# Optimization experiments

Measured on AMD Instinct MI355X. Metric: run time of the kernel, lower is better.

Reference implementation:

```python
import jax, jax.numpy as jnp
from jax import lax
import numpy as np

L, D, HEADS, DH, FF = 12, 768, 12, 64, 3072
PATCH, IMG, B, S, OUT = 16, 224, 32, 197, 512


def setup_inputs() -> dict:
    key = jax.random.key(0)
    ks = jax.random.split(key, 10)
    nrm = lambda k, shp, s=0.02: jax.random.normal(k, shp, jnp.float32) * s
    return {
        "x_inp": jax.random.normal(ks[0], (B, 3, IMG, IMG), jnp.float32),
        "conv_w": nrm(ks[1], (D, 3, PATCH, PATCH)),
        "cls_emb": nrm(ks[2], (D,)),
        "pos_emb": nrm(ks[3], (S, D)),
        "ln_pre_w": jnp.ones((D,), jnp.float32),
        "ln_pre_b": jnp.zeros((D,), jnp.float32),
        "ln1_w": jnp.ones((L, D), jnp.float32),
        "ln1_b": jnp.zeros((L, D), jnp.float32),
        "qkv_w": nrm(ks[4], (L, 3 * D, D)),
        "qkv_b": jnp.zeros((L, 3 * D), jnp.float32),
        "out_w": nrm(ks[5], (L, D, D)),
        "out_b": jnp.zeros((L, D), jnp.float32),
        "ln2_w": jnp.ones((L, D), jnp.float32),
        "ln2_b": jnp.zeros((L, D), jnp.float32),
        "fc1_w": nrm(ks[6], (L, FF, D)),
        "fc1_b": jnp.zeros((L, FF), jnp.float32),
        "fc2_w": nrm(ks[7], (L, D, FF)),
        "fc2_b": jnp.zeros((L, D), jnp.float32),
        "ln_post_w": jnp.ones((D,), jnp.float32),
        "ln_post_b": jnp.zeros((D,), jnp.float32),
        "proj": nrm(ks[8], (D, OUT)),
    }


def _ln(x, w, b, eps=1e-5):
    mu = jnp.mean(x, axis=-1, keepdims=True)
    var = jnp.mean(jnp.square(x - mu), axis=-1, keepdims=True)
    return (x - mu) * lax.rsqrt(var + eps) * w + b


def _visual_forward(x_inp, conv_w, cls_emb, pos_emb, ln_pre_w, ln_pre_b,
                    ln1_w, ln1_b, qkv_w, qkv_b, out_w, out_b,
                    ln2_w, ln2_b, fc1_w, fc1_b, fc2_w, fc2_b,
                    ln_post_w, ln_post_b, proj):
    # patch embedding: conv stride=patch, no bias  -> [B, D, 14, 14]
    x = lax.conv_general_dilated(x_inp, conv_w, (PATCH, PATCH), 'VALID',
                                 dimension_numbers=('NCHW', 'OIHW', 'NCHW'))
    b = x.shape[0]
    x = x.reshape(b, D, -1).transpose(0, 2, 1)              # [B, 196, D]
    cls = jnp.broadcast_to(cls_emb, (b, 1, D))
    x = jnp.concatenate([cls, x], axis=1)                   # [B, 197, D]
    x = x + pos_emb[None]                                   # standard 197-token branch
    x = _ln(x, ln_pre_w, ln_pre_b)

    scale = float(DH) ** -0.5

    def block(h, p):
        l1w, l1b, qw, qb, ow, ob, l2w, l2b, f1w, f1b, f2w, f2b = p
        y = _ln(h, l1w, l1b)
        qkv = y @ qw.T + qb                                  # [B, S, 3D]
        q, k, v = jnp.split(qkv, 3, axis=-1)
        q = q.reshape(b, S, HEADS, DH) * scale
        k = k.reshape(b, S, HEADS, DH)
        v = v.reshape(b, S, HEADS, DH)
        attn = jnp.einsum('bqhd,bkhd->bhqk', q, k)
        attn = jax.nn.softmax(attn, axis=-1)
        o = jnp.einsum('bhqk,bkhd->bqhd', attn, v).reshape(b, S, D)
        h = h + o @ ow.T + ob
        y = _ln(h, l2w, l2b)
        y = y @ f1w.T + f1b
        y = y * jax.nn.sigmoid(1.702 * y)                    # QuickGELU
        h = h + y @ f2w.T + f2b
        return h, None

    params = (ln1_w, ln1_b, qkv_w, qkv_b, out_w, out_b,
              ln2_w, ln2_b, fc1_w, fc1_b, fc2_w, fc2_b)
    x, _ = lax.scan(block, x, params)

    cls_out = _ln(x[:, 0, :], ln_post_w, ln_post_b)
    return cls_out @ proj                                    # [B, 512]


def reference(x_inp, conv_w, cls_emb, pos_emb, ln_pre_w, ln_pre_b,
              ln1_w, ln1_b, qkv_w, qkv_b, out_w, out_b,
              ln2_w, ln2_b, fc1_w, fc1_b, fc2_w, fc2_b,
              ln_post_w, ln_post_b, proj):
    return _visual_forward(x_inp, conv_w, cls_emb, pos_emb, ln_pre_w, ln_pre_b,
                           ln1_w, ln1_b, qkv_w, qkv_b, out_w, out_b,
                           ln2_w, ln2_b, fc1_w, fc1_b, fc2_w, fc2_b,
                           ln_post_w, ln_post_b, proj)
```

## Files before the change

kernel.cpp:

```cpp
#include <hip/hip_runtime.h>
#include <hip/hip_bf16.h>


#define LAYERS 12
#define DMODEL 768
#define NHEADS 12
#define DHEAD  64
#define FFDIM  3072
#define BATCH  32
#define SEQ    197
#define NPATCH 196
#define OUTD   512
#define MROWS  (BATCH * SEQ)
#define MPAD   6400
#define SPAD   208
#define VSTR   208

typedef __attribute__((ext_vector_type(4))) float f32x4;
typedef __attribute__((ext_vector_type(8))) short bf16x8;

enum { M_F32 = 0, M_ACC = 1, M_GELU = 2, M_PATCH = 3, M_QKVB = 4 };

__device__ __forceinline__ float b2f(short s) {
    unsigned u = ((unsigned)(unsigned short)s) << 16;
    return __builtin_bit_cast(float, u);
}
__device__ __forceinline__ short f2b(float f) {
    __hip_bfloat16 h = __float2bfloat16(f);
    return __builtin_bit_cast(short, h);
}
__device__ __forceinline__ unsigned short f2bu(float f) {
    __hip_bfloat16 h = __float2bfloat16(f);
    return __builtin_bit_cast(unsigned short, h);
}

__device__ __forceinline__ void gl2lds16(const void* g, void* l) {
    __builtin_amdgcn_global_load_lds(
        (const __attribute__((address_space(1))) void*)g,
        (__attribute__((address_space(3))) void*)l, 16, 0, 0);
}

__global__ __launch_bounds__(256) void cvt_bf16_kernel(
    const float* __restrict__ src, __hip_bfloat16* __restrict__ dst, long n)
{
    long i0 = ((long)blockIdx.x * 256 + threadIdx.x) * 4;
    long stride = (long)gridDim.x * 1024;
    for (long i = i0; i < n; i += stride) {
        float4 v = *reinterpret_cast<const float4*>(&src[i]);
        dst[i + 0] = __float2bfloat16(v.x);
        dst[i + 1] = __float2bfloat16(v.y);
        dst[i + 2] = __float2bfloat16(v.z);
        dst[i + 3] = __float2bfloat16(v.w);
    }
}

__global__ __launch_bounds__(256) void im2col_kernel(
    const float* __restrict__ x_inp, __hip_bfloat16* __restrict__ patches)
{
    int bp = blockIdx.x;
    int b = bp / NPATCH, p = bp % NPATCH;
    int py = p / 14, px = p % 14;
    const float* xb = x_inp + (long)b * 3 * 224 * 224;
    for (int e = threadIdx.x; e < 768; e += 256) {
        int c = e >> 8, i = (e >> 4) & 15, j = e & 15;
        patches[(long)bp * 768 + e] =
            __float2bfloat16(xb[((long)c * 224 + py * 16 + i) * 224 + px * 16 + j]);
    }
}

__global__ __launch_bounds__(256) void cls_token_kernel(
    const float* __restrict__ cls_emb, const float* __restrict__ pos_emb,
    float* __restrict__ x)
{
    int b = blockIdx.x;
    for (int d = threadIdx.x; d < DMODEL; d += 256)
        x[(long)b * SEQ * DMODEL + d] = cls_emb[d] + pos_emb[d];
}

template<int OB>
__global__ __launch_bounds__(256) void ln_kernel(
    const float* __restrict__ in, void* __restrict__ out,
    const float* __restrict__ w, const float* __restrict__ bb,
    long in_stride, long out_stride, int nrows)
{
    int row = blockIdx.x * 4 + (threadIdx.x >> 6);
    if (row >= nrows) return;
    int lane = threadIdx.x & 63;
    const float* xr = in + (long)row * in_stride;

    float4 v[3];
    float s = 0.f;
    #pragma unroll
    for (int i = 0; i < 3; ++i) {
        v[i] = *reinterpret_cast<const float4*>(&xr[i * 256 + lane * 4]);
        s += v[i].x + v[i].y + v[i].z + v[i].w;
    }
    #pragma unroll
    for (int off = 32; off; off >>= 1) s += __shfl_xor(s, off);
    float mean = s * (1.0f / DMODEL);
    float sq = 0.f;
    #pragma unroll
    for (int i = 0; i < 3; ++i) {
        float a = v[i].x - mean, b2 = v[i].y - mean,
              c = v[i].z - mean, d = v[i].w - mean;
        sq += a * a + b2 * b2 + c * c + d * d;
    }
    #pragma unroll
    for (int off = 32; off; off >>= 1) sq += __shfl_xor(sq, off);
    float rstd = rsqrtf(sq * (1.0f / DMODEL) + 1e-5f);

    #pragma unroll
    for (int i = 0; i < 3; ++i) {
        int d0 = i * 256 + lane * 4;
        float4 wv = *reinterpret_cast<const float4*>(&w[d0]);
        float4 bv = *reinterpret_cast<const float4*>(&bb[d0]);
        float o0 = (v[i].x - mean) * rstd * wv.x + bv.x;
        float o1 = (v[i].y - mean) * rstd * wv.y + bv.y;
        float o2 = (v[i].z - mean) * rstd * wv.z + bv.z;
        float o3 = (v[i].w - mean) * rstd * wv.w + bv.w;
        if (OB) {
            ushort4 u;
            u.x = f2bu(o0); u.y = f2bu(o1); u.z = f2bu(o2); u.w = f2bu(o3);
            *reinterpret_cast<ushort4*>(
                &((__hip_bfloat16*)out)[(long)row * out_stride + d0]) = u;
        } else {
            float4 o = make_float4(o0, o1, o2, o3);
            *reinterpret_cast<float4*>(&((float*)out)[(long)row * out_stride + d0]) = o;
        }
    }
}

template<int MODE>
__global__ __launch_bounds__(256) void gemm_bf16(
    const __hip_bfloat16* __restrict__ A, const __hip_bfloat16* __restrict__ W,
    const float* __restrict__ bias, float* __restrict__ Cf,
    __hip_bfloat16* __restrict__ Cb, int M, int N, int K, int NB,
    const float* __restrict__ pos)
{
    __shared__ short As[2][64 * 64];
    __shared__ short Bs[2][128 * 64];
    int tid = threadIdx.x, lane = tid & 63, wv = tid >> 6;

    int nwg = gridDim.x, bid = blockIdx.x;
    int qq = nwg >> 3, rr = nwg & 7;
    int xcd = bid & 7, idx = bid >> 3;
    int newid = (xcd < rr ? xcd * (qq + 1) : rr * (qq + 1) + (xcd - rr) * qq) + idx;

    int bm = (newid / NB) * 64, bn = (newid % NB) * 128;
    int wn = wv * 32;
    f32x4 acc[4][2] = {};

    int sr = tid >> 3, sc = tid & 7;
    int c_log = sc ^ (sr & 7);
    const short* Ag = (const short*)A + (long)(bm + sr) * K + (c_log << 3);
    const short* Bg = (const short*)W + (long)(bn + sr) * K + (c_log << 3);
    const long K32 = (long)32 * K;

    int lg = lane >> 4, lr16 = lane & 15;
    int aoff[2][4], boff[2][2];
    #pragma unroll
    for (int s = 0; s < 2; ++s) {
        #pragma unroll
        for (int i = 0; i < 4; ++i) {
            int ra = i * 16 + lr16;
            aoff[s][i] = (ra << 6) + ((((s << 2) | lg) ^ (ra & 7)) << 3);
        }
        #pragma unroll
        for (int j = 0; j < 2; ++j) {
            int rb = wn + j * 16 + lr16;
            boff[s][j] = (rb << 6) + ((((s << 2) | lg) ^ (rb & 7)) << 3);
        }
    }

    const int KT = K >> 6;
    {
        char* Ad = (char*)&As[0][0]; char* Bd = (char*)&Bs[0][0];
        gl2lds16(Ag,           Ad + tid * 16);
        gl2lds16(Ag + K32,     Ad + 4096 + tid * 16);
        gl2lds16(Bg,           Bd + tid * 16);
        gl2lds16(Bg + K32,     Bd + 4096 + tid * 16);
        gl2lds16(Bg + 2 * K32, Bd + 8192 + tid * 16);
        gl2lds16(Bg + 3 * K32, Bd + 12288 + tid * 16);
    }
    __syncthreads();

    for (int t = 0; t < KT; ++t) {
        if (t + 1 < KT) {
            int ktn = (t + 1) << 6;
            char* Ad = (char*)&As[(t & 1) ^ 1][0];
            char* Bd = (char*)&Bs[(t & 1) ^ 1][0];
            gl2lds16(Ag + ktn,           Ad + tid * 16);
            gl2lds16(Ag + K32 + ktn,     Ad + 4096 + tid * 16);
            gl2lds16(Bg + ktn,           Bd + tid * 16);
            gl2lds16(Bg + K32 + ktn,     Bd + 4096 + tid * 16);
            gl2lds16(Bg + 2 * K32 + ktn, Bd + 8192 + tid * 16);
            gl2lds16(Bg + 3 * K32 + ktn, Bd + 12288 + tid * 16);
        }
        const short* Ab = &As[t & 1][0];
        const short* Bb = &Bs[t & 1][0];
        #pragma unroll
        for (int s = 0; s < 2; ++s) {
            bf16x8 af[4], bfr[2];
            #pragma unroll
            for (int i = 0; i < 4; ++i)
                af[i] = *reinterpret_cast<const bf16x8*>(&Ab[aoff[s][i]]);
            #pragma unroll
            for (int j = 0; j < 2; ++j)
                bfr[j] = *reinterpret_cast<const bf16x8*>(&Bb[boff[s][j]]);
            #pragma unroll
            for (int mi = 0; mi < 4; ++mi)
                #pragma unroll
                for (int ni = 0; ni < 2; ++ni)
                    acc[mi][ni] = __builtin_amdgcn_mfma_f32_16x16x32_bf16(
                        af[mi], bfr[ni], acc[mi][ni], 0, 0, 0);
        }
        __syncthreads();
    }

    #pragma unroll
    for (int mi = 0; mi < 4; ++mi) {
        int row0 = bm + mi * 16 + (lane >> 4) * 4;
        #pragma unroll
        for (int ni = 0; ni < 2; ++ni) {
            int col = bn + wn + ni * 16 + lr16;
            #pragma unroll
            for (int r = 0; r < 4; ++r) {
                int row = row0 + r;
                if (row >= M) continue;
                float v = acc[mi][ni][r];
                if (MODE == M_PATCH) {
                    int pb = row / 196, pp = row - pb * 196;
                    Cf[((long)(pb * SEQ + 1 + pp)) * DMODEL + col] =
                        v + pos[(long)(1 + pp) * DMODEL + col];
                } else {
                    v += bias[col];
                    long idx2 = (long)row * N + col;
                    if (MODE == M_F32)      Cf[idx2] = v;
                    else if (MODE == M_ACC) Cf[idx2] += v;
                    else if (MODE == M_QKVB) Cb[idx2] = __float2bfloat16(v);
                    else if (MODE == M_GELU)
                        Cb[idx2] = __float2bfloat16(v / (1.f + __expf(-1.702f * v)));
                }
            }
        }
    }
}

__global__ __launch_bounds__(256) void attn_kernel(
    const __hip_bfloat16* __restrict__ qkv, __hip_bfloat16* __restrict__ o)
{
    int bh = blockIdx.x;
    int b = bh / NHEADS, h = bh % NHEADS;
    int tid = threadIdx.x, lane = tid & 63, wv = tid >> 6;
    __shared__ short Ks[SPAD * 64];
    __shared__ short Vt[64 * VSTR];
    __shared__ short Ps[4][16 * VSTR];
    const short* base = (const short*)qkv + (long)b * SEQ * 2304;

    for (int idx = tid; idx < SPAD * 8; idx += 256) {
        int r = idx >> 3, c = idx & 7;
        int4 val = make_int4(0, 0, 0, 0);
        if (r < SEQ)
            val = *reinterpret_cast<const int4*>(base + (long)r * 2304 + 768 + h * 64 + c * 8);
        *reinterpret_cast<int4*>(&Ks[r * 64 + ((c ^ (r & 7)) << 3)]) = val;
    }
    for (int idx = tid; idx < SPAD * 64; idx += 256) {
        int k = idx >> 6, d = idx & 63;
        short v = (k < SEQ) ? base[(long)k * 2304 + 1536 + h * 64 + d] : (short)0;
        Vt[d * VSTR + k] = v;
    }
    __syncthreads();

    int lg = lane >> 4, lr = lane & 15;
    short* Pw = Ps[wv];

    for (int ch = wv; ch < 13; ch += 4) {
        int q0 = ch * 16;
        const short* qp = (const short*)qkv +
            ((long)(b * SEQ) + q0 + lr) * 2304 + h * 64 + (lg << 3);
        bf16x8 qa = *reinterpret_cast<const bf16x8*>(qp);
        bf16x8 qb = *reinterpret_cast<const bf16x8*>(qp + 32);

        f32x4 sc[13];
        #pragma unroll
        for (int f = 0; f < 13; ++f) sc[f] = (f32x4){0.f, 0.f, 0.f, 0.f};
        #pragma unroll
        for (int f = 0; f < 13; ++f) {
            int row = f * 16 + lr;
            int sw = row & 7;
            const short* kr = &Ks[row * 64];
            bf16x8 k0 = *reinterpret_cast<const bf16x8*>(&kr[((lg + 0) ^ sw) << 3]);
            bf16x8 k1 = *reinterpret_cast<const bf16x8*>(&kr[((lg + 4) ^ sw) << 3]);
            sc[f] = __builtin_amdgcn_mfma_f32_16x16x32_bf16(qa, k0, sc[f], 0, 0, 0);
            sc[f] = __builtin_amdgcn_mfma_f32_16x16x32_bf16(qb, k1, sc[f], 0, 0, 0);
        }

        float mrow[4] = {-1e30f, -1e30f, -1e30f, -1e30f};
        #pragma unroll
        for (int f = 0; f < 13; ++f) {
            bool ok = f * 16 + lr < SEQ;
            #pragma unroll
            for (int r = 0; r < 4; ++r)
                if (ok) mrow[r] = fmaxf(mrow[r], sc[f][r] * 0.125f);
        }
        #pragma unroll
        for (int r = 0; r < 4; ++r)
            #pragma unroll
            for (int off = 8; off; off >>= 1)
                mrow[r] = fmaxf(mrow[r], __shfl_xor(mrow[r], off));
        float esum[4] = {0.f, 0.f, 0.f, 0.f};
        #pragma unroll
        for (int f = 0; f < 13; ++f) {
            bool ok = f * 16 + lr < SEQ;
            #pragma unroll
            for (int r = 0; r < 4; ++r) {
                float e = ok ? __expf(sc[f][r] * 0.125f - mrow[r]) : 0.f;
                sc[f][r] = e;
                esum[r] += e;
            }
        }
        #pragma unroll
        for (int r = 0; r < 4; ++r)
            #pragma unroll
            for (int off = 8; off; off >>= 1)
                esum[r] += __shfl_xor(esum[r], off);
        float inv[4];
        #pragma unroll
        for (int r = 0; r < 4; ++r) inv[r] = 1.0f / esum[r];

        #pragma unroll
        for (int f = 0; f < 13; ++f)
            #pragma unroll
            for (int r = 0; r < 4; ++r)
                Pw[(lg * 4 + r) * VSTR + f * 16 + lr] = f2b(sc[f][r] * inv[r]);

        f32x4 oa[4] = {};
        #pragma unroll
        for (int ks = 0; ks < 7; ++ks) {
            int kb = ks * 32 + (lg << 3);
            bf16x8 pa = {};
            if (kb < SPAD) pa = *reinterpret_cast<const bf16x8*>(&Pw[lr * VSTR + kb]);
            #pragma unroll
            for (int d = 0; d < 4; ++d) {
                bf16x8 vb = {};
                if (kb < SPAD)
                    vb = *reinterpret_cast<const bf16x8*>(&Vt[(d * 16 + lr) * VSTR + kb]);
                oa[d] = __builtin_amdgcn_mfma_f32_16x16x32_bf16(pa, vb, oa[d], 0, 0, 0);
            }
        }

        #pragma unroll
        for (int d = 0; d < 4; ++d)
            #pragma unroll
            for (int r = 0; r < 4; ++r) {
                int q = q0 + lg * 4 + r;
                if (q < SEQ)
                    o[((long)(b * SEQ + q)) * DMODEL + h * 64 + d * 16 + lr] =
                        __float2bfloat16(oa[d][r]);
            }
    }
}

__global__ __launch_bounds__(256) void proj_kernel(
    const float* __restrict__ cls_ln, const float* __restrict__ proj,
    float* __restrict__ out)
{
    int idx = blockIdx.x * 256 + threadIdx.x;
    int m = idx >> 9, n = idx & 511;
    float s = 0.f;
    #pragma unroll 8
    for (int k = 0; k < 768; ++k)
        s += cls_ln[m * 768 + k] * proj[k * 512 + n];
    out[idx] = s;
}

extern "C" void kernel_launch(void* const* d_in, const int* in_sizes, int n_in,
                              void* d_out, int out_size, void* d_ws, size_t ws_size,
                              hipStream_t stream) {
    const float* x_inp    = (const float*)d_in[0];
    const float* conv_w   = (const float*)d_in[1];
    const float* cls_emb  = (const float*)d_in[2];
    const float* pos_emb  = (const float*)d_in[3];
    const float* ln_pre_w = (const float*)d_in[4];
    const float* ln_pre_b = (const float*)d_in[5];
    const float* ln1_w    = (const float*)d_in[6];
    const float* ln1_b    = (const float*)d_in[7];
    const float* qkv_w    = (const float*)d_in[8];
    const float* qkv_b    = (const float*)d_in[9];
    const float* out_w    = (const float*)d_in[10];
    const float* out_b    = (const float*)d_in[11];
    const float* ln2_w    = (const float*)d_in[12];
    const float* ln2_b    = (const float*)d_in[13];
    const float* fc1_w    = (const float*)d_in[14];
    const float* fc1_b    = (const float*)d_in[15];
    const float* fc2_w    = (const float*)d_in[16];
    const float* fc2_b    = (const float*)d_in[17];
    const float* ln_post_w= (const float*)d_in[18];
    const float* ln_post_b= (const float*)d_in[19];
    const float* proj     = (const float*)d_in[20];

    char* w = (char*)d_ws;
    __hip_bfloat16* wqkv = (__hip_bfloat16*)w; w += (size_t)LAYERS * 2304 * DMODEL * 2;
    __hip_bfloat16* wout = (__hip_bfloat16*)w; w += (size_t)LAYERS * DMODEL * DMODEL * 2;
    __hip_bfloat16* wfc1 = (__hip_bfloat16*)w; w += (size_t)LAYERS * FFDIM * DMODEL * 2;
    __hip_bfloat16* wfc2 = (__hip_bfloat16*)w; w += (size_t)LAYERS * DMODEL * FFDIM * 2;
    __hip_bfloat16* wconv= (__hip_bfloat16*)w; w += (size_t)DMODEL * DMODEL * 2;
    float* x             = (float*)w;          w += (size_t)MROWS * DMODEL * 4;
    __hip_bfloat16* y    = (__hip_bfloat16*)w; w += (size_t)MPAD * DMODEL * 2;
    __hip_bfloat16* qkvb = (__hip_bfloat16*)w; w += (size_t)MPAD * 2304 * 2;
    __hip_bfloat16* attno= (__hip_bfloat16*)w; w += (size_t)MPAD * DMODEL * 2;
    __hip_bfloat16* h1   = (__hip_bfloat16*)w; w += (size_t)MPAD * FFDIM * 2;
    __hip_bfloat16* patches = (__hip_bfloat16*)w; w += (size_t)NPATCH * BATCH * DMODEL * 2;
    float* clsb          = (float*)w;          w += (size_t)BATCH * DMODEL * 4;

    cvt_bf16_kernel<<<2048, 256, 0, stream>>>(qkv_w, wqkv, (long)LAYERS * 2304 * DMODEL);
    cvt_bf16_kernel<<<2048, 256, 0, stream>>>(out_w, wout, (long)LAYERS * DMODEL * DMODEL);
    cvt_bf16_kernel<<<2048, 256, 0, stream>>>(fc1_w, wfc1, (long)LAYERS * FFDIM * DMODEL);
    cvt_bf16_kernel<<<2048, 256, 0, stream>>>(fc2_w, wfc2, (long)LAYERS * DMODEL * FFDIM);
    cvt_bf16_kernel<<<512, 256, 0, stream>>>(conv_w, wconv, (long)DMODEL * DMODEL);

    im2col_kernel<<<NPATCH * BATCH, 256, 0, stream>>>(x_inp, patches);
    gemm_bf16<M_PATCH><<<98 * 6, 256, 0, stream>>>(
        patches, wconv, nullptr, x, nullptr, NPATCH * BATCH, DMODEL, DMODEL, 6, pos_emb);
    cls_token_kernel<<<BATCH, 256, 0, stream>>>(cls_emb, pos_emb, x);
    ln_kernel<0><<<MROWS / 4, 256, 0, stream>>>(x, x, ln_pre_w, ln_pre_b,
                                                DMODEL, DMODEL, MROWS);

    for (int l = 0; l < LAYERS; ++l) {
        ln_kernel<1><<<MROWS / 4, 256, 0, stream>>>(x, y, ln1_w + l * DMODEL,
                                                    ln1_b + l * DMODEL, DMODEL, DMODEL, MROWS);
        gemm_bf16<M_QKVB><<<99 * 18, 256, 0, stream>>>(
            y, wqkv + (long)l * 2304 * DMODEL, qkv_b + (long)l * 2304, nullptr, qkvb,
            MROWS, 2304, DMODEL, 18, nullptr);
        attn_kernel<<<BATCH * NHEADS, 256, 0, stream>>>(qkvb, attno);
        gemm_bf16<M_ACC><<<99 * 6, 256, 0, stream>>>(
            attno, wout + (long)l * DMODEL * DMODEL, out_b + (long)l * DMODEL, x, nullptr,
            MROWS, DMODEL, DMODEL, 6, nullptr);
        ln_kernel<1><<<MROWS / 4, 256, 0, stream>>>(x, y, ln2_w + l * DMODEL,
                                                    ln2_b + l * DMODEL, DMODEL, DMODEL, MROWS);
        gemm_bf16<M_GELU><<<99 * 24, 256, 0, stream>>>(
            y, wfc1 + (long)l * FFDIM * DMODEL, fc1_b + (long)l * FFDIM, nullptr, h1,
            MROWS, FFDIM, DMODEL, 24, nullptr);
        gemm_bf16<M_ACC><<<99 * 6, 256, 0, stream>>>(
            h1, wfc2 + (long)l * DMODEL * FFDIM, fc2_b + (long)l * DMODEL, x, nullptr,
            MROWS, DMODEL, FFDIM, 6, nullptr);
    }

    ln_kernel<0><<<8, 256, 0, stream>>>(x, clsb, ln_post_w, ln_post_b,
                                        (long)SEQ * DMODEL, DMODEL, BATCH);
    proj_kernel<<<(BATCH * OUTD) / 256, 256, 0, stream>>>(clsb, proj, (float*)d_out);
}
```

Baseline: 3.404 ms.

## Add 128x128-tile GEMM with XCD-aware block remap for QKV and FC1

Adds a gemm128 kernel that uses 128x128 output tiles with a 64-wide K step, XOR-swizzled LDS and direct global-to-LDS loads. It also remaps block IDs so consecutive tiles land on the same XCD. The QKV and FC1 projections now use it in place of the previous 64-row-tile GEMM. The goal is more data reuse per loaded tile and better L2 locality on the large-N GEMMs. The trade-off is fewer workgroups, padding waste at M=6304 against 6400 rows, and higher register pressure from a 4x4 accumulator per wave.

```diff
diff --git a/kernel.cpp b/kernel.cpp
--- a/kernel.cpp
+++ b/kernel.cpp
@@ -241,6 +241,93 @@
                     else if (MODE == M_GELU)
                         Cb[idx2] = __float2bfloat16(v / (1.f + __expf(-1.702f * v)));
                 }
+            }
+        }
+    }
+}
+
+template<int MODE>
+__global__ __launch_bounds__(256) void gemm128(
+    const __hip_bfloat16* __restrict__ A, const __hip_bfloat16* __restrict__ W,
+    const float* __restrict__ bias, __hip_bfloat16* __restrict__ Cb,
+    int M, int N, int K, int NB)
+{
+    __shared__ short As[128 * 64];
+    __shared__ short Bs[128 * 64];
+    int tid = threadIdx.x, lane = tid & 63, wv = tid >> 6;
+
+    int nwg = gridDim.x, bid = blockIdx.x;
+    int qq = nwg >> 3, rr = nwg & 7;
+    int xcd = bid & 7, idx = bid >> 3;
+    int newid = (xcd < rr ? xcd * (qq + 1) : rr * (qq + 1) + (xcd - rr) * qq) + idx;
+
+    int bm = (newid / NB) * 128, bn = (newid % NB) * 128;
+    int wr = wv >> 1, wc = wv & 1;
+    f32x4 acc[4][4] = {};
+
+    int sr = tid >> 3, scn = tid & 7;
+    int c_log = scn ^ (sr & 7);
+    const short* Ag = (const short*)A + (long)(bm + sr) * K + (c_log << 3);
+    const short* Bg = (const short*)W + (long)(bn + sr) * K + (c_log << 3);
+    const long K32 = (long)32 * K;
+
+    int lg = lane >> 4, lr16 = lane & 15;
+    int aoff[2][4], boff[2][4];
+    #pragma unroll
+    for (int s = 0; s < 2; ++s) {
+        int kc = (s << 2) | lg;
+        #pragma unroll
+        for (int i = 0; i < 4; ++i) {
+            int ra = wr * 64 + i * 16 + lr16;
+            aoff[s][i] = (ra << 6) + ((kc ^ (ra & 7)) << 3);
+            int rb = wc * 64 + i * 16 + lr16;
+            boff[s][i] = (rb << 6) + ((kc ^ (rb & 7)) << 3);
+        }
+    }
+
+    const int KT = K >> 6;
+    for (int t = 0; t < KT; ++t) {
+        if (t) __syncthreads();
+        int kt = t << 6;
+        #pragma unroll
+        for (int p = 0; p < 4; ++p) {
+            gl2lds16(Ag + p * K32 + kt, (char*)As + p * 4096 + tid * 16);
+            gl2lds16(Bg + p * K32 + kt, (char*)Bs + p * 4096 + tid * 16);
+        }
+        __syncthreads();
+
+        #pragma unroll
+        for (int s = 0; s < 2; ++s) {
+            bf16x8 af[4], bfr[4];
+            #pragma unroll
+            for (int i = 0; i < 4; ++i)
+                af[i] = *reinterpret_cast<const bf16x8*>(&As[aoff[s][i]]);
+            #pragma unroll
+            for (int j = 0; j < 4; ++j)
+                bfr[j] = *reinterpret_cast<const bf16x8*>(&Bs[boff[s][j]]);
+            #pragma unroll
+            for (int mi = 0; mi < 4; ++mi)
+                #pragma unroll
+                for (int ni = 0; ni < 4; ++ni)
+                    acc[mi][ni] = __builtin_amdgcn_mfma_f32_16x16x32_bf16(
+                        af[mi], bfr[ni], acc[mi][ni], 0, 0, 0);
+        }
+    }
+
+    #pragma unroll
+    for (int mi = 0; mi < 4; ++mi) {
+        int row0 = bm + wr * 64 + mi * 16 + lg * 4;
+        #pragma unroll
+        for (int ni = 0; ni < 4; ++ni) {
+            int col = bn + wc * 64 + ni * 16 + lr16;
+            #pragma unroll
+            for (int r = 0; r < 4; ++r) {
+                int row = row0 + r;
+                if (row >= M) continue;
+                float v = acc[mi][ni][r] + bias[col];
+                long idx2 = (long)row * N + col;
+                if (MODE == M_QKVB) Cb[idx2] = __float2bfloat16(v);
+                else                Cb[idx2] = __float2bfloat16(v / (1.f + __expf(-1.702f * v)));
             }
         }
     }
@@ -429,18 +516,18 @@
     for (int l = 0; l < LAYERS; ++l) {
         ln_kernel<1><<<MROWS / 4, 256, 0, stream>>>(x, y, ln1_w + l * DMODEL,
                                                     ln1_b + l * DMODEL, DMODEL, DMODEL, MROWS);
-        gemm_bf16<M_QKVB><<<99 * 18, 256, 0, stream>>>(
-            y, wqkv + (long)l * 2304 * DMODEL, qkv_b + (long)l * 2304, nullptr, qkvb,
-            MROWS, 2304, DMODEL, 18, nullptr);
+        gemm128<M_QKVB><<<50 * 18, 256, 0, stream>>>(
+            y, wqkv + (long)l * 2304 * DMODEL, qkv_b + (long)l * 2304, qkvb,
+            MROWS, 2304, DMODEL, 18);
         attn_kernel<<<BATCH * NHEADS, 256, 0, stream>>>(qkvb, attno);
         gemm_bf16<M_ACC><<<99 * 6, 256, 0, stream>>>(
             attno, wout + (long)l * DMODEL * DMODEL, out_b + (long)l * DMODEL, x, nullptr,
             MROWS, DMODEL, DMODEL, 6, nullptr);
         ln_kernel<1><<<MROWS / 4, 256, 0, stream>>>(x, y, ln2_w + l * DMODEL,
                                                     ln2_b + l * DMODEL, DMODEL, DMODEL, MROWS);
-        gemm_bf16<M_GELU><<<99 * 24, 256, 0, stream>>>(
-            y, wfc1 + (long)l * FFDIM * DMODEL, fc1_b + (long)l * FFDIM, nullptr, h1,
-            MROWS, FFDIM, DMODEL, 24, nullptr);
+        gemm128<M_GELU><<<50 * 24, 256, 0, stream>>>(
+            y, wfc1 + (long)l * FFDIM * DMODEL, fc1_b + (long)l * FFDIM, h1,
+            MROWS, FFDIM, DMODEL, 24);
         gemm_bf16<M_ACC><<<99 * 6, 256, 0, stream>>>(
             h1, wfc2 + (long)l * DMODEL * FFDIM, fc2_b + (long)l * DMODEL, x, nullptr,
             MROWS, DMODEL, FFDIM, 6, nullptr);
```

Result: faster. 3.182 ms (-6.5%).
